# Optimization experiments

Hardware: AMD Instinct MI355X
Metric: run time of the kernel (lower is better)

## Reference

```python
import jax, jax.numpy as jnp
import numpy as np

EPS = 1e-3  # keras LayerNormalization default epsilon

def _layernorm(x, g, b):
    mu = jnp.mean(x, axis=-1, keepdims=True)
    var = jnp.mean(jnp.square(x - mu), axis=-1, keepdims=True)
    return (x - mu) * jax.lax.rsqrt(var + EPS) * g + b

def setup_inputs() -> dict:
    key = jax.random.key(0)
    ks = jax.random.split(key, 12)
    B, T, C = 2, 2048, 768
    s = 0.02
    return {
        "x": jax.random.normal(ks[0], (B, T, C), jnp.float32),
        "ln1_g": jnp.ones((C,), jnp.float32), "ln1_b": jnp.zeros((C,), jnp.float32),
        "Wq": jax.random.normal(ks[1], (C, C), jnp.float32) * s, "bq": jnp.zeros((C,), jnp.float32),
        "Wk": jax.random.normal(ks[2], (C, C), jnp.float32) * s, "bk": jnp.zeros((C,), jnp.float32),
        "Wv": jax.random.normal(ks[3], (C, C), jnp.float32) * s, "bv": jnp.zeros((C,), jnp.float32),
        "ln2_g": jnp.ones((C,), jnp.float32), "ln2_b": jnp.zeros((C,), jnp.float32),
        "W1": jax.random.normal(ks[4], (C, 4 * C), jnp.float32) * s, "b1": jnp.zeros((4 * C,), jnp.float32),
        "W2": jax.random.normal(ks[5], (4 * C, C), jnp.float32) * s, "b2": jnp.zeros((C,), jnp.float32),
    }

def reference(x, ln1_g, ln1_b, Wq, bq, Wk, bk, Wv, bv, ln2_g, ln2_b, W1, b1, W2, b2):
    H = 12
    B, T, C = x.shape
    dh = C // H
    # pre-LN (note: original overwrites x with LN output before residual)
    x = _layernorm(x, ln1_g, ln1_b)
    q = (x @ Wq + bq).reshape(B, T, H, dh).transpose(0, 2, 1, 3)
    k = (x @ Wk + bk).reshape(B, T, H, dh).transpose(0, 2, 1, 3)
    v = (x @ Wv + bv).reshape(B, T, H, dh).transpose(0, 2, 1, 3)
    # original computes K @ Q^T (transpose_b on query)
    scores = jnp.einsum('bhid,bhjd->bhij', k, q) / jnp.sqrt(jnp.float32(dh))
    mask = jnp.tril(jnp.ones((T, T), bool))
    scores = jnp.where(mask, scores, -jnp.inf)
    p = jax.nn.softmax(scores, axis=-1)
    y = jnp.einsum('bhij,bhjd->bhid', p, v)  # [B,H,T,dh]
    y = y.transpose(0, 2, 1, 3).reshape(B, T, C)
    x = x + y
    h = _layernorm(x, ln2_g, ln2_b)
    h = jax.nn.gelu(h @ W1 + b1, approximate=False)
    h = h @ W2 + b2
    return x + h
```

## Files before the change

kernel.cpp:

```cpp
#include <hip/hip_runtime.h>
#include <hip/hip_bf16.h>
#include <cmath>


#define BB 2
#define TT 2048
#define CC 768
#define HH 12
#define DH 64
#define NROWS (BB*TT)

typedef __attribute__((ext_vector_type(8))) short bf16x8;
typedef __attribute__((ext_vector_type(4))) float f32x4;
typedef __attribute__((ext_vector_type(4))) unsigned short u16x4;

__device__ __forceinline__ unsigned short f2bf(float f){
  union { __hip_bfloat16 h; unsigned short u; } c;
  c.h = __float2bfloat16(f);
  return c.u;
}
__device__ __forceinline__ int swz(int r, int c){
  int b = (r << 7) + (c << 1);
  b ^= (r & 7) << 4;
  return b >> 1;
}
__device__ __forceinline__ float wred_sum(float v){
  #pragma unroll
  for(int m = 1; m < 64; m <<= 1) v += __shfl_xor(v, m, 64);
  return v;
}
__device__ __forceinline__ float gelu_exact(float x){
  return 0.5f * x * (1.0f + erff(x * 0.70710678118654752f));
}
__device__ __forceinline__ void gload_lds16(const void* g, void* l){
  __builtin_amdgcn_global_load_lds((const __attribute__((address_space(1))) void*)g,
                                   (__attribute__((address_space(3))) void*)l, 16, 0, 0);
}
template<int N> __device__ __forceinline__ void waitcnt_vm(){
  if constexpr (N == 0)      asm volatile("s_waitcnt vmcnt(0)" ::: "memory");
  else if constexpr (N == 4) asm volatile("s_waitcnt vmcnt(4)" ::: "memory");
  else if constexpr (N == 8) asm volatile("s_waitcnt vmcnt(8)" ::: "memory");
  else static_assert(N == 0 || N == 4 || N == 8, "unsupported vmcnt");
}

__global__ __launch_bounds__(256) void transpose_convert(const float* __restrict__ in,
                                                         unsigned short* __restrict__ out,
                                                         int K, int N){
  __shared__ float tile[32][33];
  int n0 = blockIdx.x * 32, k0 = blockIdx.y * 32;
  int t = threadIdx.x; int c = t & 31; int r0 = t >> 5;
  #pragma unroll
  for(int p = 0; p < 4; p++){
    int r = r0 + p * 8;
    tile[r][c] = in[(size_t)(k0 + r) * N + n0 + c];
  }
  __syncthreads();
  #pragma unroll
  for(int p = 0; p < 4; p++){
    int r = r0 + p * 8;
    out[(size_t)(n0 + r) * K + k0 + c] = f2bf(tile[c][r]);
  }
}

__global__ __launch_bounds__(256) void transpose_convert_qkv(const float* __restrict__ Wq,
                                                             const float* __restrict__ Wk,
                                                             const float* __restrict__ Wv,
                                                             unsigned short* __restrict__ out){
  __shared__ float tile[32][33];
  const float* in = (blockIdx.z == 0) ? Wq : (blockIdx.z == 1) ? Wk : Wv;
  unsigned short* o = out + (size_t)blockIdx.z * CC * CC;
  int n0 = blockIdx.x * 32, k0 = blockIdx.y * 32;
  int t = threadIdx.x; int c = t & 31; int r0 = t >> 5;
  #pragma unroll
  for(int p = 0; p < 4; p++){
    int r = r0 + p * 8;
    tile[r][c] = in[(size_t)(k0 + r) * CC + n0 + c];
  }
  __syncthreads();
  #pragma unroll
  for(int p = 0; p < 4; p++){
    int r = r0 + p * 8;
    o[(size_t)(n0 + r) * CC + k0 + c] = f2bf(tile[c][r]);
  }
}

__global__ __launch_bounds__(256) void concat_bias(const float* __restrict__ bq,
                                                   const float* __restrict__ bk,
                                                   const float* __restrict__ bv,
                                                   float* __restrict__ bqkv){
  int i = blockIdx.x * 256 + threadIdx.x;
  if(i < 3 * CC) bqkv[i] = (i < CC) ? bq[i] : (i < 2 * CC) ? bk[i - CC] : bv[i - 2 * CC];
}

__global__ __launch_bounds__(256) void ln_kernel(const float* __restrict__ in,
                                                 const float* __restrict__ gm,
                                                 const float* __restrict__ bt,
                                                 float* __restrict__ out_f,
                                                 unsigned short* __restrict__ out_b){
  int r = blockIdx.x; int t = threadIdx.x;
  const float* row = in + (size_t)r * CC;
  float v0 = row[t], v1 = row[t + 256], v2 = row[t + 512];
  float s = wred_sum(v0 + v1 + v2);
  __shared__ float red[4];
  if((t & 63) == 0) red[t >> 6] = s;
  __syncthreads();
  float mu = (red[0] + red[1] + red[2] + red[3]) * (1.0f / CC);
  float d0 = v0 - mu, d1 = v1 - mu, d2 = v2 - mu;
  float q = wred_sum(d0 * d0 + d1 * d1 + d2 * d2);
  __shared__ float red2[4];
  if((t & 63) == 0) red2[t >> 6] = q;
  __syncthreads();
  float var = (red2[0] + red2[1] + red2[2] + red2[3]) * (1.0f / CC);
  float rinv = rsqrtf(var + 1e-3f);
  float o0 = d0 * rinv * gm[t]       + bt[t];
  float o1 = d1 * rinv * gm[t + 256] + bt[t + 256];
  float o2 = d2 * rinv * gm[t + 512] + bt[t + 512];
  size_t base = (size_t)r * CC;
  if(out_f){ out_f[base + t] = o0; out_f[base + t + 256] = o1; out_f[base + t + 512] = o2; }
  out_b[base + t] = f2bf(o0); out_b[base + t + 256] = f2bf(o1); out_b[base + t + 512] = f2bf(o2);
}

template<int MODE, int TILE>
__global__ __launch_bounds__(256) void gemm_bt(const unsigned short* __restrict__ A,
                                               const unsigned short* __restrict__ Bt,
                                               const float* __restrict__ bias,
                                               const float* __restrict__ resid,
                                               void* __restrict__ outp,
                                               int M, int N, int K){
  constexpr int F = TILE / 32;
  constexpr int R = TILE / 32;
  constexpr int NLD = 2 * R;
  __shared__ unsigned short As[2][TILE * 64];
  __shared__ unsigned short Bs[2][TILE * 64];
  int m0 = blockIdx.y * TILE, n0 = blockIdx.x * TILE;
  int t = threadIdx.x; int w = t >> 6; int l = t & 63;
  int g = l >> 4; int lc = l & 15;
  int wm = w >> 1, wn = w & 1;
  f32x4 zero4 = {0.f, 0.f, 0.f, 0.f};
  f32x4 acc[F][F];
  #pragma unroll
  for(int mi = 0; mi < F; mi++)
    #pragma unroll
    for(int ni = 0; ni < F; ni++) acc[mi][ni] = zero4;

  auto stage = [&](int ks, int cb){
    #pragma unroll
    for(int p = 0; p < R; p++){
      int e = (w * R + p) * 512 + l * 8;
      int r = e >> 6, clin = e & 63;
      int csrc = clin ^ ((r & 7) << 3);
      gload_lds16(A  + (size_t)(m0 + r) * K + ks + csrc, &As[cb][(w * R + p) * 512]);
      gload_lds16(Bt + (size_t)(n0 + r) * K + ks + csrc, &Bs[cb][(w * R + p) * 512]);
    }
  };

  int nt = K >> 6;
  stage(0, 0);
  if(nt > 1) stage(64, 1);
  for(int ti = 0; ti < nt; ti++){
    if(ti + 1 < nt) waitcnt_vm<NLD>(); else waitcnt_vm<0>();
    __builtin_amdgcn_s_barrier();
    int cur = ti & 1;
    #pragma unroll
    for(int kk = 0; kk < 2; kk++){
      bf16x8 af[F], bfv[F];
      #pragma unroll
      for(int mi = 0; mi < F; mi++) af[mi]  = *(const bf16x8*)&As[cur][swz(wm * (TILE / 2) + mi * 16 + lc, kk * 32 + g * 8)];
      #pragma unroll
      for(int ni = 0; ni < F; ni++) bfv[ni] = *(const bf16x8*)&Bs[cur][swz(wn * (TILE / 2) + ni * 16 + lc, kk * 32 + g * 8)];
      #pragma unroll
      for(int mi = 0; mi < F; mi++)
        #pragma unroll
        for(int ni = 0; ni < F; ni++)
          acc[mi][ni] = __builtin_amdgcn_mfma_f32_16x16x32_bf16(af[mi], bfv[ni], acc[mi][ni], 0, 0, 0);
    }
    __builtin_amdgcn_s_barrier();
    if(ti + 2 < nt) stage((ti + 2) << 6, cur);
  }
  #pragma unroll
  for(int mi = 0; mi < F; mi++)
    #pragma unroll
    for(int ni = 0; ni < F; ni++){
      int col = n0 + wn * (TILE / 2) + ni * 16 + lc;
      float bvv = bias[col];
      #pragma unroll
      for(int rr = 0; rr < 4; rr++){
        int row = m0 + wm * (TILE / 2) + mi * 16 + g * 4 + rr;
        float v = acc[mi][ni][rr] + bvv;
        size_t idx = (size_t)row * N + col;
        if(MODE == 1) v = gelu_exact(v);
        if(MODE == 2) ((float*)outp)[idx] = v + resid[idx];
        else          ((unsigned short*)outp)[idx] = f2bf(v);
      }
    }
}

__global__ __launch_bounds__(256) void transpose_v(const unsigned short* __restrict__ qkv,
                                                   unsigned short* __restrict__ vt){
  __shared__ unsigned short tile[64][65];
  int t0 = blockIdx.x * 64; int bh = blockIdx.y;
  int b = bh / HH, h = bh % HH;
  int t = threadIdx.x;
  #pragma unroll
  for(int p = 0; p < 2; p++){
    int idx = p * 256 + t; int r = idx >> 3; int c = (idx & 7) * 8;
    bf16x8 v = *(const bf16x8*)(qkv + (size_t)(b * TT + t0 + r) * (3 * CC) + 2 * CC + h * DH + c);
    #pragma unroll
    for(int e = 0; e < 8; e++) tile[r][c + e] = (unsigned short)v[e];
  }
  __syncthreads();
  #pragma unroll
  for(int p = 0; p < 2; p++){
    int idx = p * 256 + t; int d = idx >> 3; int c = (idx & 7) * 8;
    bf16x8 v;
    #pragma unroll
    for(int e = 0; e < 8; e++) v[e] = (short)tile[c + e][d];
    *(bf16x8*)(vt + (size_t)(bh * DH + d) * TT + t0 + c) = v;
  }
}

__global__ __launch_bounds__(256) void attn_kernel(const unsigned short* __restrict__ qkv,
                                                   const unsigned short* __restrict__ vt,
                                                   const float* __restrict__ xln,
                                                   float* __restrict__ x1){
  __shared__ unsigned short Aq[2][64 * 64];
  __shared__ unsigned short Vs[2][64 * 64];
  __shared__ unsigned short Ps[4][16 * 64];
  int o = blockIdx.x;
  int xcd = o & 7, qq = o >> 3;
  int head = xcd * 3 + (qq % 3);
  int bx = 31 - qq / 3;
  int b = head / HH, h = head % HH;
  int t = threadIdx.x; int w = t >> 6; int l = t & 63;
  int g = l >> 4, lc = l & 15;
  int i0w = bx * 64 + w * 16;
  int irow = i0w + lc;
  unsigned short* pw = &Ps[w][0];
  const float SC = 0.125f * 1.44269504f;

  int rl = l >> 3;
  int csrc = ((l & 7) * 8) ^ (rl * 8);

  bf16x8 bk[2];
  #pragma unroll
  for(int kk = 0; kk < 2; kk++)
    bk[kk] = *(const bf16x8*)(qkv + (size_t)(b * TT + irow) * (3 * CC) + CC + h * DH + kk * 32 + g * 8);

  float m_ = 0.0f, lsum = 0.f;
  f32x4 zero4 = {0.f, 0.f, 0.f, 0.f};
  f32x4 o4[4];
  #pragma unroll
  for(int ds = 0; ds < 4; ds++) o4[ds] = zero4;

  int NJT_w = (i0w + 16 + 63) >> 6;
  int NJTmax = bx + 1;

  auto stage = [&](int j0, int cb){
    #pragma unroll
    for(int p = 0; p < 2; p++){
      int sgi = w * 2 + p;
      int row = sgi * 8 + rl;
      gload_lds16(qkv + (size_t)(b * TT + j0 + row) * (3 * CC) + h * DH + csrc, &Aq[cb][sgi * 512]);
      gload_lds16(vt  + (size_t)(head * DH + row) * TT + j0 + csrc,             &Vs[cb][sgi * 512]);
    }
  };

  stage(0, 0);
  if(NJTmax > 1) stage(64, 1);

  for(int jt = 0; jt < NJTmax; jt++){
    int j0 = jt * 64;
    int buf = jt & 1;
    if(jt + 1 < NJTmax) waitcnt_vm<4>(); else waitcnt_vm<0>();
    __builtin_amdgcn_s_barrier();
    if(jt < NJT_w){
      f32x4 s[4];
      __builtin_amdgcn_s_setprio(1);
      #pragma unroll
      for(int js = 0; js < 4; js++){
        s[js] = zero4;
        #pragma unroll
        for(int kk = 0; kk < 2; kk++){
          bf16x8 aq = *(const bf16x8*)&Aq[buf][swz(js * 16 + lc, kk * 32 + g * 8)];
          s[js] = __builtin_amdgcn_mfma_f32_16x16x32_bf16(aq, bk[kk], s[js], 0, 0, 0);
        }
      }
      __builtin_amdgcn_s_setprio(0);
      if(j0 + 63 > i0w){
        #pragma unroll
        for(int js = 0; js < 4; js++)
          #pragma unroll
          for(int rr = 0; rr < 4; rr++){
            int j = j0 + js * 16 + g * 4 + rr;
            if(j > irow) s[js][rr] = -1e30f;
          }
      }
      float nmSC = -m_ * SC;
      f32x4 p[4];
      float rsum = 0.f;
      #pragma unroll
      for(int js = 0; js < 4; js++)
        #pragma unroll
        for(int rr = 0; rr < 4; rr++){
          float pv = exp2f(fmaf(s[js][rr], SC, nmSC));
          p[js][rr] = pv;
          rsum += pv;
        }
      rsum += __shfl_xor(rsum, 16, 64);
      rsum += __shfl_xor(rsum, 32, 64);
      if(__builtin_expect(__any(!(rsum < 1e30f)), 0)){
        float mx = -1e30f;
        #pragma unroll
        for(int js = 0; js < 4; js++)
          #pragma unroll
          for(int rr = 0; rr < 4; rr++) mx = fmaxf(mx, s[js][rr]);
        mx = fmaxf(mx, __shfl_xor(mx, 16, 64));
        mx = fmaxf(mx, __shfl_xor(mx, 32, 64));
        float mn = fmaxf(m_, mx);
        float al = exp2f((m_ - mn) * SC);
        m_ = mn;
        lsum *= al;
        #pragma unroll
        for(int rr = 0; rr < 4; rr++){
          float alb = __shfl(al, g * 4 + rr, 64);
          #pragma unroll
          for(int ds = 0; ds < 4; ds++) o4[ds][rr] *= alb;
        }
        nmSC = -m_ * SC;
        rsum = 0.f;
        #pragma unroll
        for(int js = 0; js < 4; js++)
          #pragma unroll
          for(int rr = 0; rr < 4; rr++){
            float pv = exp2f(fmaf(s[js][rr], SC, nmSC));
            p[js][rr] = pv;
            rsum += pv;
          }
        rsum += __shfl_xor(rsum, 16, 64);
        rsum += __shfl_xor(rsum, 32, 64);
      }
      lsum += rsum;
      #pragma unroll
      for(int js = 0; js < 4; js++){
        u16x4 pk;
        #pragma unroll
        for(int rr = 0; rr < 4; rr++) pk[rr] = f2bf(p[js][rr]);
        *(u16x4*)&pw[swz(lc, js * 16 + g * 4)] = pk;
      }
      bf16x8 pa[2];
      #pragma unroll
      for(int kk = 0; kk < 2; kk++)
        pa[kk] = *(const bf16x8*)&pw[swz(lc, kk * 32 + g * 8)];
      __builtin_amdgcn_s_setprio(1);
      #pragma unroll
      for(int ds = 0; ds < 4; ds++)
        #pragma unroll
        for(int kk = 0; kk < 2; kk++){
          bf16x8 vb = *(const bf16x8*)&Vs[buf][swz(ds * 16 + lc, kk * 32 + g * 8)];
          o4[ds] = __builtin_amdgcn_mfma_f32_16x16x32_bf16(pa[kk], vb, o4[ds], 0, 0, 0);
        }
      __builtin_amdgcn_s_setprio(0);
    }
    __builtin_amdgcn_s_barrier();
    if(jt + 2 < NJTmax) stage((jt + 2) * 64, buf);
  }
  #pragma unroll
  for(int rr = 0; rr < 4; rr++){
    float lsb = __shfl(lsum, g * 4 + rr, 64);
    float rinv = 1.0f / lsb;
    int ig = i0w + g * 4 + rr;
    #pragma unroll
    for(int ds = 0; ds < 4; ds++){
      int col = h * DH + ds * 16 + lc;
      size_t idx = (size_t)(b * TT + ig) * CC + col;
      x1[idx] = xln[idx] + o4[ds][rr] * rinv;
    }
  }
}

extern "C" void kernel_launch(void* const* d_in, const int* in_sizes, int n_in,
                              void* d_out, int out_size, void* d_ws, size_t ws_size,
                              hipStream_t stream){
  const float* x    = (const float*)d_in[0];
  const float* ln1g = (const float*)d_in[1];
  const float* ln1b = (const float*)d_in[2];
  const float* Wq   = (const float*)d_in[3];
  const float* bq   = (const float*)d_in[4];
  const float* Wk   = (const float*)d_in[5];
  const float* bk   = (const float*)d_in[6];
  const float* Wv   = (const float*)d_in[7];
  const float* bv   = (const float*)d_in[8];
  const float* ln2g = (const float*)d_in[9];
  const float* ln2b = (const float*)d_in[10];
  const float* W1   = (const float*)d_in[11];
  const float* b1   = (const float*)d_in[12];
  const float* W2   = (const float*)d_in[13];
  const float* b2   = (const float*)d_in[14];

  char* ws = (char*)d_ws;
  float*          xlnf = (float*)(ws + 0);
  unsigned short* xlnb = (unsigned short*)(ws + 12582912);
  float*          x1   = (float*)(ws + 18874368);
  unsigned short* hln2 = (unsigned short*)(ws + 31457280);
  unsigned short* wqkv = (unsigned short*)(ws + 37748736);
  float*          bqkv = (float*)(ws + 41287680);
  unsigned short* w1t  = (unsigned short*)(ws + 41296896);
  unsigned short* w2t  = (unsigned short*)(ws + 46015488);
  unsigned short* qkv  = (unsigned short*)(ws + 50734080);
  unsigned short* vt   = (unsigned short*)(ws + 69608448);
  unsigned short* mlp1 = (unsigned short*)(ws + 50734080);

  transpose_convert_qkv<<<dim3(24, 24, 3), 256, 0, stream>>>(Wq, Wk, Wv, wqkv);
  transpose_convert<<<dim3(96, 24), 256, 0, stream>>>(W1, w1t, CC, 4 * CC);
  transpose_convert<<<dim3(24, 96), 256, 0, stream>>>(W2, w2t, 4 * CC, CC);
  concat_bias<<<9, 256, 0, stream>>>(bq, bk, bv, bqkv);

  ln_kernel<<<NROWS, 256, 0, stream>>>(x, ln1g, ln1b, xlnf, xlnb);

  gemm_bt<0, 128><<<dim3(18, 32), 256, 0, stream>>>(xlnb, wqkv, bqkv, nullptr, qkv, NROWS, 3 * CC, CC);

  transpose_v<<<dim3(TT / 64, BB * HH), 256, 0, stream>>>(qkv, vt);

  attn_kernel<<<dim3(768), 256, 0, stream>>>(qkv, vt, xlnf, x1);

  ln_kernel<<<NROWS, 256, 0, stream>>>(x1, ln2g, ln2b, nullptr, hln2);

  gemm_bt<1, 128><<<dim3(24, 32), 256, 0, stream>>>(hln2, w1t, b1, nullptr, mlp1, NROWS, 4 * CC, CC);

  gemm_bt<2, 64><<<dim3(12, 64), 256, 0, stream>>>(mlp1, w2t, b2, x1, d_out, NROWS, CC, 4 * CC);

  (void)in_sizes; (void)n_in; (void)out_size; (void)ws_size;
}
```

Baseline: 183.3 us.

## Process two query tiles per attention block and merge weight-prep launches

Each attention block now handles 128 rows instead of 64, split into two 64-row sub-tiles that share every staged K/V tile. This halves the grid and the global-to-LDS staging traffic per row. The four weight transpose and bias-concat kernels are folded into one launch to cut launch overhead. The fp32 LayerNorm output is no longer written, so the attention residual is rebuilt from the bf16 copy. That lowers residual precision, and the doubled register state and coarser grid may hurt occupancy and load balance.

```diff
diff --git a/kernel.cpp b/kernel.cpp
--- a/kernel.cpp
+++ b/kernel.cpp
@@ -19,6 +19,9 @@
   c.h = __float2bfloat16(f);
   return c.u;
 }
+__device__ __forceinline__ float bf2f(unsigned short u){
+  union { unsigned int i; float f; } x; x.i = ((unsigned int)u) << 16; return x.f;
+}
 __device__ __forceinline__ int swz(int r, int c){
   int b = (r << 7) + (c << 1);
   b ^= (r & 7) << 4;
@@ -43,11 +46,11 @@
   else static_assert(N == 0 || N == 4 || N == 8, "unsupported vmcnt");
 }
 
-__global__ __launch_bounds__(256) void transpose_convert(const float* __restrict__ in,
-                                                         unsigned short* __restrict__ out,
-                                                         int K, int N){
-  __shared__ float tile[32][33];
-  int n0 = blockIdx.x * 32, k0 = blockIdx.y * 32;
+__device__ __forceinline__ void tc_body(const float* __restrict__ in,
+                                        unsigned short* __restrict__ out,
+                                        int K, int N, int bx, int by,
+                                        float (*tile)[33]){
+  int n0 = bx * 32, k0 = by * 32;
   int t = threadIdx.x; int c = t & 31; int r0 = t >> 5;
   #pragma unroll
   for(int p = 0; p < 4; p++){
@@ -62,40 +65,39 @@
   }
 }
 
-__global__ __launch_bounds__(256) void transpose_convert_qkv(const float* __restrict__ Wq,
-                                                             const float* __restrict__ Wk,
-                                                             const float* __restrict__ Wv,
-                                                             unsigned short* __restrict__ out){
-  __shared__ float tile[32][33];
-  const float* in = (blockIdx.z == 0) ? Wq : (blockIdx.z == 1) ? Wk : Wv;
-  unsigned short* o = out + (size_t)blockIdx.z * CC * CC;
-  int n0 = blockIdx.x * 32, k0 = blockIdx.y * 32;
-  int t = threadIdx.x; int c = t & 31; int r0 = t >> 5;
-  #pragma unroll
-  for(int p = 0; p < 4; p++){
-    int r = r0 + p * 8;
-    tile[r][c] = in[(size_t)(k0 + r) * CC + n0 + c];
-  }
-  __syncthreads();
-  #pragma unroll
-  for(int p = 0; p < 4; p++){
-    int r = r0 + p * 8;
-    o[(size_t)(n0 + r) * CC + k0 + c] = f2bf(tile[c][r]);
-  }
-}
-
-__global__ __launch_bounds__(256) void concat_bias(const float* __restrict__ bq,
+__global__ __launch_bounds__(256) void prep_kernel(const float* __restrict__ Wq,
+                                                   const float* __restrict__ Wk,
+                                                   const float* __restrict__ Wv,
+                                                   const float* __restrict__ W1,
+                                                   const float* __restrict__ W2,
+                                                   const float* __restrict__ bq,
                                                    const float* __restrict__ bk,
                                                    const float* __restrict__ bv,
+                                                   unsigned short* __restrict__ wqkv,
+                                                   unsigned short* __restrict__ w1t,
+                                                   unsigned short* __restrict__ w2t,
                                                    float* __restrict__ bqkv){
-  int i = blockIdx.x * 256 + threadIdx.x;
-  if(i < 3 * CC) bqkv[i] = (i < CC) ? bq[i] : (i < 2 * CC) ? bk[i - CC] : bv[i - 2 * CC];
+  __shared__ float tile[32][33];
+  int o = blockIdx.x;
+  if(o < 1728){
+    int z = o / 576, r = o % 576;
+    const float* in = (z == 0) ? Wq : (z == 1) ? Wk : Wv;
+    tc_body(in, wqkv + (size_t)z * CC * CC, CC, CC, r % 24, r / 24, tile);
+  } else if(o < 4032){
+    int r = o - 1728;
+    tc_body(W1, w1t, CC, 4 * CC, r % 96, r / 96, tile);
+  } else if(o < 6336){
+    int r = o - 4032;
+    tc_body(W2, w2t, 4 * CC, CC, r % 24, r / 24, tile);
+  } else {
+    int i = (o - 6336) * 256 + threadIdx.x;
+    if(i < 3 * CC) bqkv[i] = (i < CC) ? bq[i] : (i < 2 * CC) ? bk[i - CC] : bv[i - 2 * CC];
+  }
 }
 
 __global__ __launch_bounds__(256) void ln_kernel(const float* __restrict__ in,
                                                  const float* __restrict__ gm,
                                                  const float* __restrict__ bt,
-                                                 float* __restrict__ out_f,
                                                  unsigned short* __restrict__ out_b){
   int r = blockIdx.x; int t = threadIdx.x;
   const float* row = in + (size_t)r * CC;
@@ -116,7 +118,6 @@
   float o1 = d1 * rinv * gm[t + 256] + bt[t + 256];
   float o2 = d2 * rinv * gm[t + 512] + bt[t + 512];
   size_t base = (size_t)r * CC;
-  if(out_f){ out_f[base + t] = o0; out_f[base + t + 256] = o1; out_f[base + t + 512] = o2; }
   out_b[base + t] = f2bf(o0); out_b[base + t + 256] = f2bf(o1); out_b[base + t + 512] = f2bf(o2);
 }
 
@@ -221,39 +222,42 @@
 
 __global__ __launch_bounds__(256) void attn_kernel(const unsigned short* __restrict__ qkv,
                                                    const unsigned short* __restrict__ vt,
-                                                   const float* __restrict__ xln,
+                                                   const unsigned short* __restrict__ xlnb,
                                                    float* __restrict__ x1){
   __shared__ unsigned short Aq[2][64 * 64];
   __shared__ unsigned short Vs[2][64 * 64];
-  __shared__ unsigned short Ps[4][16 * 64];
+  __shared__ unsigned short Ps[4][2 * 16 * 64];
   int o = blockIdx.x;
   int xcd = o & 7, qq = o >> 3;
   int head = xcd * 3 + (qq % 3);
-  int bx = 31 - qq / 3;
+  int bx = 15 - qq / 3;
   int b = head / HH, h = head % HH;
   int t = threadIdx.x; int w = t >> 6; int l = t & 63;
   int g = l >> 4, lc = l & 15;
-  int i0w = bx * 64 + w * 16;
-  int irow = i0w + lc;
-  unsigned short* pw = &Ps[w][0];
+  int i0A = bx * 128 + w * 16;
+  int i0B = i0A + 64;
+  int irowA = i0A + lc, irowB = i0B + lc;
+  unsigned short* pwA = &Ps[w][0];
+  unsigned short* pwB = &Ps[w][1024];
   const float SC = 0.125f * 1.44269504f;
 
   int rl = l >> 3;
   int csrc = ((l & 7) * 8) ^ (rl * 8);
 
-  bf16x8 bk[2];
-  #pragma unroll
-  for(int kk = 0; kk < 2; kk++)
-    bk[kk] = *(const bf16x8*)(qkv + (size_t)(b * TT + irow) * (3 * CC) + CC + h * DH + kk * 32 + g * 8);
-
-  float m_ = 0.0f, lsum = 0.f;
+  bf16x8 bkA[2], bkB[2];
+  #pragma unroll
+  for(int kk = 0; kk < 2; kk++){
+    bkA[kk] = *(const bf16x8*)(qkv + (size_t)(b * TT + irowA) * (3 * CC) + CC + h * DH + kk * 32 + g * 8);
+    bkB[kk] = *(const bf16x8*)(qkv + (size_t)(b * TT + irowB) * (3 * CC) + CC + h * DH + kk * 32 + g * 8);
+  }
+
+  float mA = 0.0f, lsumA = 0.f, mB = 0.0f, lsumB = 0.f;
   f32x4 zero4 = {0.f, 0.f, 0.f, 0.f};
-  f32x4 o4[4];
-  #pragma unroll
-  for(int ds = 0; ds < 4; ds++) o4[ds] = zero4;
-
-  int NJT_w = (i0w + 16 + 63) >> 6;
-  int NJTmax = bx + 1;
+  f32x4 oA[4], oB[4];
+  #pragma unroll
+  for(int ds = 0; ds < 4; ds++){ oA[ds] = zero4; oB[ds] = zero4; }
+
+  int NJTmax = 2 * bx + 2;
 
   auto stage = [&](int j0, int cb){
     #pragma unroll
@@ -271,109 +275,225 @@
   for(int jt = 0; jt < NJTmax; jt++){
     int j0 = jt * 64;
     int buf = jt & 1;
+    bool doA   = (jt < NJTmax - 1);
+    bool maskA = (jt == NJTmax - 2);
+    bool maskB = (jt == NJTmax - 1);
     if(jt + 1 < NJTmax) waitcnt_vm<4>(); else waitcnt_vm<0>();
     __builtin_amdgcn_s_barrier();
-    if(jt < NJT_w){
-      f32x4 s[4];
-      __builtin_amdgcn_s_setprio(1);
+
+    f32x4 sA[4], sB[4];
+    __builtin_amdgcn_s_setprio(1);
+    if(doA){
       #pragma unroll
       for(int js = 0; js < 4; js++){
-        s[js] = zero4;
+        sA[js] = zero4;
         #pragma unroll
         for(int kk = 0; kk < 2; kk++){
           bf16x8 aq = *(const bf16x8*)&Aq[buf][swz(js * 16 + lc, kk * 32 + g * 8)];
-          s[js] = __builtin_amdgcn_mfma_f32_16x16x32_bf16(aq, bk[kk], s[js], 0, 0, 0);
-        }
-      }
-      __builtin_amdgcn_s_setprio(0);
-      if(j0 + 63 > i0w){
+          sA[js] = __builtin_amdgcn_mfma_f32_16x16x32_bf16(aq, bkA[kk], sA[js], 0, 0, 0);
+        }
+      }
+    }
+    #pragma unroll
+    for(int js = 0; js < 4; js++){
+      sB[js] = zero4;
+      #pragma unroll
+      for(int kk = 0; kk < 2; kk++){
+        bf16x8 aq = *(const bf16x8*)&Aq[buf][swz(js * 16 + lc, kk * 32 + g * 8)];
+        sB[js] = __builtin_amdgcn_mfma_f32_16x16x32_bf16(aq, bkB[kk], sB[js], 0, 0, 0);
+      }
+    }
+    __builtin_amdgcn_s_setprio(0);
+
+    if(maskA){
+      #pragma unroll
+      for(int js = 0; js < 4; js++)
+        #pragma unroll
+        for(int rr = 0; rr < 4; rr++){
+          int j = j0 + js * 16 + g * 4 + rr;
+          if(j > irowA) sA[js][rr] = -1e30f;
+        }
+    }
+    if(maskB){
+      #pragma unroll
+      for(int js = 0; js < 4; js++)
+        #pragma unroll
+        for(int rr = 0; rr < 4; rr++){
+          int j = j0 + js * 16 + g * 4 + rr;
+          if(j > irowB) sB[js][rr] = -1e30f;
+        }
+    }
+
+    float rsumA = 0.f, rsumB = 0.f;
+    {
+      float nmA = -mA * SC, nmB = -mB * SC;
+      if(doA){
         #pragma unroll
         for(int js = 0; js < 4; js++)
           #pragma unroll
           for(int rr = 0; rr < 4; rr++){
-            int j = j0 + js * 16 + g * 4 + rr;
-            if(j > irow) s[js][rr] = -1e30f;
+            float pv = exp2f(fmaf(sA[js][rr], SC, nmA));
+            sA[js][rr] = pv; rsumA += pv;
           }
       }
-      float nmSC = -m_ * SC;
-      f32x4 p[4];
-      float rsum = 0.f;
       #pragma unroll
       for(int js = 0; js < 4; js++)
         #pragma unroll
         for(int rr = 0; rr < 4; rr++){
-          float pv = exp2f(fmaf(s[js][rr], SC, nmSC));
-          p[js][rr] = pv;
-          rsum += pv;
-        }
-      rsum += __shfl_xor(rsum, 16, 64);
-      rsum += __shfl_xor(rsum, 32, 64);
-      if(__builtin_expect(__any(!(rsum < 1e30f)), 0)){
+          float pv = exp2f(fmaf(sB[js][rr], SC, nmB));
+          sB[js][rr] = pv; rsumB += pv;
+        }
+      rsumA += __shfl_xor(rsumA, 16, 64); rsumA += __shfl_xor(rsumA, 32, 64);
+      rsumB += __shfl_xor(rsumB, 16, 64); rsumB += __shfl_xor(rsumB, 32, 64);
+    }
+    if(__builtin_expect(__any(!(rsumA < 1e30f) || !(rsumB < 1e30f)), 0)){
+      if(doA){
+        f32x4 raw[4];
+        #pragma unroll
+        for(int js = 0; js < 4; js++){
+          raw[js] = zero4;
+          #pragma unroll
+          for(int kk = 0; kk < 2; kk++){
+            bf16x8 aq = *(const bf16x8*)&Aq[buf][swz(js * 16 + lc, kk * 32 + g * 8)];
+            raw[js] = __builtin_amdgcn_mfma_f32_16x16x32_bf16(aq, bkA[kk], raw[js], 0, 0, 0);
+          }
+        }
+        if(maskA){
+          #pragma unroll
+          for(int js = 0; js < 4; js++)
+            #pragma unroll
+            for(int rr = 0; rr < 4; rr++){
+              int j = j0 + js * 16 + g * 4 + rr;
+              if(j > irowA) raw[js][rr] = -1e30f;
+            }
+        }
         float mx = -1e30f;
         #pragma unroll
         for(int js = 0; js < 4; js++)
           #pragma unroll
-          for(int rr = 0; rr < 4; rr++) mx = fmaxf(mx, s[js][rr]);
+          for(int rr = 0; rr < 4; rr++) mx = fmaxf(mx, raw[js][rr]);
         mx = fmaxf(mx, __shfl_xor(mx, 16, 64));
         mx = fmaxf(mx, __shfl_xor(mx, 32, 64));
-        float mn = fmaxf(m_, mx);
-        float al = exp2f((m_ - mn) * SC);
-        m_ = mn;
-        lsum *= al;
+        float mn = fmaxf(mA, mx);
+        float al = exp2f((mA - mn) * SC);
+        mA = mn; lsumA *= al;
         #pragma unroll
         for(int rr = 0; rr < 4; rr++){
           float alb = __shfl(al, g * 4 + rr, 64);
           #pragma unroll
-          for(int ds = 0; ds < 4; ds++) o4[ds][rr] *= alb;
-        }
-        nmSC = -m_ * SC;
-        rsum = 0.f;
+          for(int ds = 0; ds < 4; ds++) oA[ds][rr] *= alb;
+        }
+        float nm = -mA * SC; rsumA = 0.f;
         #pragma unroll
         for(int js = 0; js < 4; js++)
           #pragma unroll
           for(int rr = 0; rr < 4; rr++){
-            float pv = exp2f(fmaf(s[js][rr], SC, nmSC));
-            p[js][rr] = pv;
-            rsum += pv;
+            float pv = exp2f(fmaf(raw[js][rr], SC, nm));
+            sA[js][rr] = pv; rsumA += pv;
           }
-        rsum += __shfl_xor(rsum, 16, 64);
-        rsum += __shfl_xor(rsum, 32, 64);
-      }
-      lsum += rsum;
+        rsumA += __shfl_xor(rsumA, 16, 64); rsumA += __shfl_xor(rsumA, 32, 64);
+      }
+      {
+        f32x4 raw[4];
+        #pragma unroll
+        for(int js = 0; js < 4; js++){
+          raw[js] = zero4;
+          #pragma unroll
+          for(int kk = 0; kk < 2; kk++){
+            bf16x8 aq = *(const bf16x8*)&Aq[buf][swz(js * 16 + lc, kk * 32 + g * 8)];
+            raw[js] = __builtin_amdgcn_mfma_f32_16x16x32_bf16(aq, bkB[kk], raw[js], 0, 0, 0);
+          }
+        }
+        if(maskB){
+          #pragma unroll
+          for(int js = 0; js < 4; js++)
+            #pragma unroll
+            for(int rr = 0; rr < 4; rr++){
+              int j = j0 + js * 16 + g * 4 + rr;
+              if(j > irowB) raw[js][rr] = -1e30f;
+            }
+        }
+        float mx = -1e30f;
+        #pragma unroll
+        for(int js = 0; js < 4; js++)
+          #pragma unroll
+          for(int rr = 0; rr < 4; rr++) mx = fmaxf(mx, raw[js][rr]);
+        mx = fmaxf(mx, __shfl_xor(mx, 16, 64));
+        mx = fmaxf(mx, __shfl_xor(mx, 32, 64));
+        float mn = fmaxf(mB, mx);
+        float al = exp2f((mB - mn) * SC);
+        mB = mn; lsumB *= al;
+        #pragma unroll
+        for(int rr = 0; rr < 4; rr++){
+          float alb = __shfl(al, g * 4 + rr, 64);
+          #pragma unroll
+          for(int ds = 0; ds < 4; ds++) oB[ds][rr] *= alb;
+        }
+        float nm = -mB * SC; rsumB = 0.f;
+        #pragma unroll
+        for(int js = 0; js < 4; js++)
+          #pragma unroll
+          for(int rr = 0; rr < 4; rr++){
+            float pv = exp2f(fmaf(raw[js][rr], SC, nm));
+            sB[js][rr] = pv; rsumB += pv;
+          }
+        rsumB += __shfl_xor(rsumB, 16, 64); rsumB += __shfl_xor(rsumB, 32, 64);
+      }
+    }
+    lsumA += rsumA; lsumB += rsumB;
+
+    if(doA){
       #pragma unroll
       for(int js = 0; js < 4; js++){
         u16x4 pk;
         #pragma unroll
-        for(int rr = 0; rr < 4; rr++) pk[rr] = f2bf(p[js][rr]);
-        *(u16x4*)&pw[swz(lc, js * 16 + g * 4)] = pk;
-      }
-      bf16x8 pa[2];
-      #pragma unroll
-      for(int kk = 0; kk < 2; kk++)
-        pa[kk] = *(const bf16x8*)&pw[swz(lc, kk * 32 + g * 8)];
-      __builtin_amdgcn_s_setprio(1);
-      #pragma unroll
-      for(int ds = 0; ds < 4; ds++)
-        #pragma unroll
-        for(int kk = 0; kk < 2; kk++){
-          bf16x8 vb = *(const bf16x8*)&Vs[buf][swz(ds * 16 + lc, kk * 32 + g * 8)];
-          o4[ds] = __builtin_amdgcn_mfma_f32_16x16x32_bf16(pa[kk], vb, o4[ds], 0, 0, 0);
-        }
-      __builtin_amdgcn_s_setprio(0);
-    }
+        for(int rr = 0; rr < 4; rr++) pk[rr] = f2bf(sA[js][rr]);
+        *(u16x4*)&pwA[swz(lc, js * 16 + g * 4)] = pk;
+      }
+    }
+    #pragma unroll
+    for(int js = 0; js < 4; js++){
+      u16x4 pk;
+      #pragma unroll
+      for(int rr = 0; rr < 4; rr++) pk[rr] = f2bf(sB[js][rr]);
+      *(u16x4*)&pwB[swz(lc, js * 16 + g * 4)] = pk;
+    }
+    bf16x8 paA[2], paB[2];
+    #pragma unroll
+    for(int kk = 0; kk < 2; kk++){
+      paA[kk] = *(const bf16x8*)&pwA[swz(lc, kk * 32 + g * 8)];
+      paB[kk] = *(const bf16x8*)&pwB[swz(lc, kk * 32 + g * 8)];
+    }
+    __builtin_amdgcn_s_setprio(1);
+    #pragma unroll
+    for(int ds = 0; ds < 4; ds++){
+      #pragma unroll
+      for(int kk = 0; kk < 2; kk++){
+        bf16x8 vb = *(const bf16x8*)&Vs[buf][swz(ds * 16 + lc, kk * 32 + g * 8)];
+        if(jt < NJTmax - 1) oA[ds] = __builtin_amdgcn_mfma_f32_16x16x32_bf16(paA[kk], vb, oA[ds], 0, 0, 0);
+        oB[ds] = __builtin_amdgcn_mfma_f32_16x16x32_bf16(paB[kk], vb, oB[ds], 0, 0, 0);
+      }
+    }
+    __builtin_amdgcn_s_setprio(0);
+
     __builtin_amdgcn_s_barrier();
     if(jt + 2 < NJTmax) stage((jt + 2) * 64, buf);
   }
   #pragma unroll
   for(int rr = 0; rr < 4; rr++){
-    float lsb = __shfl(lsum, g * 4 + rr, 64);
-    float rinv = 1.0f / lsb;
-    int ig = i0w + g * 4 + rr;
+    float lsbA = __shfl(lsumA, g * 4 + rr, 64);
+    float lsbB = __shfl(lsumB, g * 4 + rr, 64);
+    float rinvA = 1.0f / lsbA;
+    float rinvB = 1.0f / lsbB;
+    int igA = i0A + g * 4 + rr;
+    int igB = i0B + g * 4 + rr;
     #pragma unroll
     for(int ds = 0; ds < 4; ds++){
       int col = h * DH + ds * 16 + lc;
-      size_t idx = (size_t)(b * TT + ig) * CC + col;
-      x1[idx] = xln[idx] + o4[ds][rr] * rinv;
+      size_t idxA = (size_t)(b * TT + igA) * CC + col;
+      size_t idxB = (size_t)(b * TT + igB) * CC + col;
+      x1[idxA] = bf2f(xlnb[idxA]) + oA[ds][rr] * rinvA;
+      x1[idxB] = bf2f(xlnb[idxB]) + oB[ds][rr] * rinvB;
     }
   }
 }
@@ -398,7 +518,6 @@
   const float* b2   = (const float*)d_in[14];
 
   char* ws = (char*)d_ws;
-  float*          xlnf = (float*)(ws + 0);
   unsigned short* xlnb = (unsigned short*)(ws + 12582912);
   float*          x1   = (float*)(ws + 18874368);
   unsigned short* hln2 = (unsigned short*)(ws + 31457280);
@@ -410,20 +529,18 @@
   unsigned short* vt   = (unsigned short*)(ws + 69608448);
   unsigned short* mlp1 = (unsigned short*)(ws + 50734080);
 
-  transpose_convert_qkv<<<dim3(24, 24, 3), 256, 0, stream>>>(Wq, Wk, Wv, wqkv);
-  transpose_convert<<<dim3(96, 24), 256, 0, stream>>>(W1, w1t, CC, 4 * CC);
-  transpose_convert<<<dim3(24, 96), 256, 0, stream>>>(W2, w2t, 4 * CC, CC);
-  concat_bias<<<9, 256, 0, stream>>>(bq, bk, bv, bqkv);
-
-  ln_kernel<<<NROWS, 256, 0, stream>>>(x, ln1g, ln1b, xlnf, xlnb);
+  prep_kernel<<<dim3(6345), 256, 0, stream>>>(Wq, Wk, Wv, W1, W2, bq, bk, bv,
+                                              wqkv, w1t, w2t, bqkv);
+
+  ln_kernel<<<NROWS, 256, 0, stream>>>(x, ln1g, ln1b, xlnb);
 
   gemm_bt<0, 128><<<dim3(18, 32), 256, 0, stream>>>(xlnb, wqkv, bqkv, nullptr, qkv, NROWS, 3 * CC, CC);
 
   transpose_v<<<dim3(TT / 64, BB * HH), 256, 0, stream>>>(qkv, vt);
 
-  attn_kernel<<<dim3(768), 256, 0, stream>>>(qkv, vt, xlnf, x1);
-
-  ln_kernel<<<NROWS, 256, 0, stream>>>(x1, ln2g, ln2b, nullptr, hln2);
+  attn_kernel<<<dim3(384), 256, 0, stream>>>(qkv, vt, xlnb, x1);
+
+  ln_kernel<<<NROWS, 256, 0, stream>>>(x1, ln2g, ln2b, hln2);
 
   gemm_bt<1, 128><<<dim3(24, 32), 256, 0, stream>>>(hln2, w1t, b1, nullptr, mlp1, NROWS, 4 * CC, CC);
 
```

New measurement: 204.9 us. 11.7% more time.
